# Kernel tuning notes

Measured on AMD Instinct MI355X. Metric: run time of the kernel, lower is better.

Reference implementation:

```python
import jax, jax.numpy as jnp
import numpy as np

CW = 32            # correlationWidth (number of disparities)
HR = 3             # horizontalCorrelationRadius
VR = 3             # verticalCorrelationRadius
EPS = 1e-09        # normalizationEpsilon
KH, KW = 2 * VR + 1, 2 * HR + 1  # unfold kernel (7,7)

B, C, H, W = 2, 16, 128, 256


def _unfold_patches(img):
    # img: [b,c,h,w] -> [b, c*KH*KW, h, w'] ('same' padding, like nn.Unfold with padding=(3,3)).
    # Feature-dim ordering differs from torch's unfold but NCC is invariant to it
    # (mean / norm / dot all reduce over the full patch dim).
    return jax.lax.conv_general_dilated_patches(
        img, (KH, KW), (1, 1), [(VR, VR), (HR, HR)])


def _normalize_patches(p):
    # zero-mean, unit-L2 per patch (reduce over feature dim 1)
    p = p - p.mean(axis=1, keepdims=True)
    return p / jnp.sqrt(jnp.sum(p * p, axis=1, keepdims=True) + EPS)


def setup_inputs() -> dict:
    key = jax.random.key(0)
    k1, k2 = jax.random.split(key)
    im_left = jax.random.normal(k1, (B, C, H, W), dtype=jnp.float32)
    im_right = jax.random.normal(k2, (B, C, H, W), dtype=jnp.float32)
    return {"im_left": im_left, "im_right": im_right}


def reference(im_left, im_right):
    b, c, h, w = im_left.shape
    # ZeroPad2d((0, CW-1, 0, 0)): pad right edge of width by CW-1 zeros
    left_ext = jnp.pad(im_left, ((0, 0), (0, 0), (0, 0), (0, CW - 1)))
    pl = _normalize_patches(_unfold_patches(left_ext))   # [b,P,h,w+CW-1]
    pr = _normalize_patches(_unfold_patches(im_right))   # [b,P,h,w]
    # cost[b,y,x,d] = <normalized left patch at (y, x+d), normalized right patch at (y, x)>
    cost = jnp.stack(
        [jnp.einsum('bpyx,bpyx->byx', pl[..., d:d + w], pr) for d in range(CW)],
        axis=-1)  # [b,h,w,CW]
    return cost
```

## Files before the change

kernel.cpp:

```cpp
#include <hip/hip_runtime.h>

#define NB 2
#define NC 16
#define NH 128
#define NW 256
#define NCW 32
#define HW (NH*NW)
#define PATCH_INV (1.0f/784.0f)
#define EPS_N 1e-9f
#define HB_W 272

__global__ __launch_bounds__(256) void ncc_kernel(
    const float* __restrict__ L, const float* __restrict__ R, float* __restrict__ out)
{
    __shared__ float csL[NW], cs2L[NW], csR[NW], cs2R[NW];
    __shared__ float sSL[288], sInvL[288], sSR[NW], sInvR[NW];
    __shared__ float hbuf[NCW][HB_W];

    const int bid = blockIdx.x;
    const int lin = (bid & 7) * 32 + (bid >> 3);
    const int b = lin >> 7;
    const int y = lin & 127;

    const int t  = threadIdx.x;
    const int dq = t >> 6;
    const int xg = t & 63;
    const int x0 = xg << 2;
    const int d0 = dq << 3;
    const int s  = x0 + d0;

    const size_t base = (size_t)b * NC * HW;

    {
        float aL = 0.f, a2L = 0.f, aR = 0.f, a2R = 0.f;
        #pragma unroll
        for (int dy = -3; dy <= 3; ++dy) {
            int yy = y + dy;
            if ((unsigned)yy < NH) {
                const float* lp = L + base + (size_t)yy * NW + t;
                const float* rp = R + base + (size_t)yy * NW + t;
                #pragma unroll
                for (int c = 0; c < NC; ++c) {
                    float lv = lp[c * HW];
                    float rv = rp[c * HW];
                    aL += lv; a2L += lv * lv;
                    aR += rv; a2R += rv * rv;
                }
            }
        }
        csL[t] = aL; cs2L[t] = a2L; csR[t] = aR; cs2R[t] = a2R;
    }
    __syncthreads();

    #pragma unroll
    for (int rep = 0; rep < 2; ++rep) {
        int xe = t + rep * 256;
        if (xe < 288) {
            float S = 0.f, S2 = 0.f;
            #pragma unroll
            for (int dx = -3; dx <= 3; ++dx) {
                int xx = xe + dx;
                if ((unsigned)xx < NW) { S += csL[xx]; S2 += cs2L[xx]; }
            }
            sSL[xe]   = S;
            sInvL[xe] = rsqrtf(S2 - S * S * PATCH_INV + EPS_N);
        }
    }
    {
        float S = 0.f, S2 = 0.f;
        #pragma unroll
        for (int dx = -3; dx <= 3; ++dx) {
            int xx = t + dx;
            if ((unsigned)xx < NW) { S += csR[xx]; S2 += cs2R[xx]; }
        }
        sSR[t]   = S;
        sInvR[t] = rsqrtf(S2 - S * S * PATCH_INV + EPS_N);
    }
    __syncthreads();

    float vp[4][8];
    #pragma unroll
    for (int i = 0; i < 4; ++i)
        #pragma unroll
        for (int j = 0; j < 8; ++j) vp[i][j] = 0.f;

    #pragma unroll
    for (int dy = -3; dy <= 3; ++dy) {
        const int yy = y + dy;
        if ((unsigned)yy < NH) {
            const float* lrow = L + base + (size_t)yy * NW;
            const float* rrow = R + base + (size_t)yy * NW;
            #pragma unroll
            for (int c = 0; c < NC; ++c) {
                const float* lc = lrow + (size_t)c * HW;
                const float* rc = rrow + (size_t)c * HW;
                float4 rv4 = *(const float4*)(rc + x0);
                float rv[4] = {rv4.x, rv4.y, rv4.z, rv4.w};
                float lw[12];
                #pragma unroll
                for (int ch = 0; ch < 3; ++ch) {
                    int col  = s + ch * 4;
                    int colc = col < (NW - 4) ? col : (NW - 4);
                    float4 lv = *(const float4*)(lc + colc);
                    bool ok = (col < NW);
                    lw[ch*4+0] = ok ? lv.x : 0.f;
                    lw[ch*4+1] = ok ? lv.y : 0.f;
                    lw[ch*4+2] = ok ? lv.z : 0.f;
                    lw[ch*4+3] = ok ? lv.w : 0.f;
                }
                #pragma unroll
                for (int xx = 0; xx < 4; ++xx)
                    #pragma unroll
                    for (int j = 0; j < 8; ++j)
                        vp[xx][j] += lw[xx + j] * rv[xx];
            }
        }
    }
    #pragma unroll
    for (int j = 0; j < 8; ++j)
        *(float4*)&hbuf[d0 + j][4 + x0] =
            make_float4(vp[0][j], vp[1][j], vp[2][j], vp[3][j]);
    if (t < 128) {
        int r = t >> 2, q = t & 3;
        int col = (q == 0) ? 0 : (260 + 4 * (q - 1));
        *(float4*)&hbuf[r][col] = make_float4(0.f, 0.f, 0.f, 0.f);
    }
    __syncthreads();

    float res[4][8];
    #pragma unroll
    for (int j = 0; j < 8; ++j) {
        float4 w0 = *(float4*)&hbuf[d0+j][x0];
        float4 w1 = *(float4*)&hbuf[d0+j][x0+4];
        float4 w2 = *(float4*)&hbuf[d0+j][x0+8];
        float w[12] = {w0.x,w0.y,w0.z,w0.w, w1.x,w1.y,w1.z,w1.w, w2.x,w2.y,w2.z,w2.w};
        #pragma unroll
        for (int xx = 0; xx < 4; ++xx) {
            float sum = 0.f;
            #pragma unroll
            for (int k = 1; k <= 7; ++k) sum += w[xx + k];
            float slv = sSL[s + xx + j];
            float ilv = sInvL[s + xx + j];
            float srv = sSR[x0 + xx];
            float irv = sInvR[x0 + xx];
            res[xx][j] = (sum - slv * srv * PATCH_INV) * ilv * irv;
        }
    }

    float* op = out + (((size_t)(b * NH + y) * NW) + x0) * NCW + d0;
    #pragma unroll
    for (int xx = 0; xx < 4; ++xx) {
        *(float4*)(op + (size_t)xx * NCW)     =
            make_float4(res[xx][0], res[xx][1], res[xx][2], res[xx][3]);
        *(float4*)(op + (size_t)xx * NCW + 4) =
            make_float4(res[xx][4], res[xx][5], res[xx][6], res[xx][7]);
    }
}

extern "C" void kernel_launch(void* const* d_in, const int* in_sizes, int n_in,
                              void* d_out, int out_size, void* d_ws, size_t ws_size,
                              hipStream_t stream) {
    const float* L = (const float*)d_in[0];
    const float* R = (const float*)d_in[1];
    float* out = (float*)d_out;
    ncc_kernel<<<dim3(NB * NH), dim3(256), 0, stream>>>(L, R, out);
}
```

Measured before the change: 84.79 us.

## Double threads per block, each computing 4 disparities instead of 8

Blocks grow to 512 threads, and each thread now handles 4 disparities per 4 x-positions instead of 8. The box-sum prologue is split so that half the threads cover the left image and half the right. This raises the number of waves per block for 256 blocks on a large GPU, giving better latency hiding and fewer registers per thread. The cost is more redundant global loads of the left and right rows per disparity group and a larger block that may limit residency.

```diff
diff --git a/kernel.cpp b/kernel.cpp
--- a/kernel.cpp
+++ b/kernel.cpp
@@ -10,7 +10,7 @@
 #define EPS_N 1e-9f
 #define HB_W 272
 
-__global__ __launch_bounds__(256) void ncc_kernel(
+__global__ __launch_bounds__(512) void ncc_kernel(
     const float* __restrict__ L, const float* __restrict__ R, float* __restrict__ out)
 {
     __shared__ float csL[NW], cs2L[NW], csR[NW], cs2R[NW];
@@ -26,63 +26,60 @@
     const int dq = t >> 6;
     const int xg = t & 63;
     const int x0 = xg << 2;
-    const int d0 = dq << 3;
+    const int d0 = dq << 2;
     const int s  = x0 + d0;
 
     const size_t base = (size_t)b * NC * HW;
 
     {
-        float aL = 0.f, a2L = 0.f, aR = 0.f, a2R = 0.f;
+        const float* img = (t < 256) ? L : R;
+        const int col = t & 255;
+        float a = 0.f, a2 = 0.f;
         #pragma unroll
         for (int dy = -3; dy <= 3; ++dy) {
             int yy = y + dy;
             if ((unsigned)yy < NH) {
-                const float* lp = L + base + (size_t)yy * NW + t;
-                const float* rp = R + base + (size_t)yy * NW + t;
+                const float* p = img + base + (size_t)yy * NW + col;
                 #pragma unroll
                 for (int c = 0; c < NC; ++c) {
-                    float lv = lp[c * HW];
-                    float rv = rp[c * HW];
-                    aL += lv; a2L += lv * lv;
-                    aR += rv; a2R += rv * rv;
+                    float v = p[c * HW];
+                    a += v; a2 += v * v;
                 }
             }
         }
-        csL[t] = aL; cs2L[t] = a2L; csR[t] = aR; cs2R[t] = a2R;
+        if (t < 256) { csL[col] = a; cs2L[col] = a2; }
+        else         { csR[col] = a; cs2R[col] = a2; }
     }
     __syncthreads();
 
-    #pragma unroll
-    for (int rep = 0; rep < 2; ++rep) {
-        int xe = t + rep * 256;
-        if (xe < 288) {
-            float S = 0.f, S2 = 0.f;
-            #pragma unroll
-            for (int dx = -3; dx <= 3; ++dx) {
-                int xx = xe + dx;
-                if ((unsigned)xx < NW) { S += csL[xx]; S2 += cs2L[xx]; }
-            }
-            sSL[xe]   = S;
-            sInvL[xe] = rsqrtf(S2 - S * S * PATCH_INV + EPS_N);
-        }
-    }
-    {
+    if (t < 288) {
         float S = 0.f, S2 = 0.f;
         #pragma unroll
         for (int dx = -3; dx <= 3; ++dx) {
             int xx = t + dx;
+            if ((unsigned)xx < NW) { S += csL[xx]; S2 += cs2L[xx]; }
+        }
+        sSL[t]   = S;
+        sInvL[t] = rsqrtf(S2 - S * S * PATCH_INV + EPS_N);
+    }
+    if (t >= 256) {
+        const int xr = t - 256;
+        float S = 0.f, S2 = 0.f;
+        #pragma unroll
+        for (int dx = -3; dx <= 3; ++dx) {
+            int xx = xr + dx;
             if ((unsigned)xx < NW) { S += csR[xx]; S2 += cs2R[xx]; }
         }
-        sSR[t]   = S;
-        sInvR[t] = rsqrtf(S2 - S * S * PATCH_INV + EPS_N);
+        sSR[xr]   = S;
+        sInvR[xr] = rsqrtf(S2 - S * S * PATCH_INV + EPS_N);
     }
     __syncthreads();
 
-    float vp[4][8];
+    float vp[4][4];
     #pragma unroll
     for (int i = 0; i < 4; ++i)
         #pragma unroll
-        for (int j = 0; j < 8; ++j) vp[i][j] = 0.f;
+        for (int j = 0; j < 4; ++j) vp[i][j] = 0.f;
 
     #pragma unroll
     for (int dy = -3; dy <= 3; ++dy) {
@@ -96,9 +93,9 @@
                 const float* rc = rrow + (size_t)c * HW;
                 float4 rv4 = *(const float4*)(rc + x0);
                 float rv[4] = {rv4.x, rv4.y, rv4.z, rv4.w};
-                float lw[12];
+                float lw[8];
                 #pragma unroll
-                for (int ch = 0; ch < 3; ++ch) {
+                for (int ch = 0; ch < 2; ++ch) {
                     int col  = s + ch * 4;
                     int colc = col < (NW - 4) ? col : (NW - 4);
                     float4 lv = *(const float4*)(lc + colc);
@@ -111,13 +108,13 @@
                 #pragma unroll
                 for (int xx = 0; xx < 4; ++xx)
                     #pragma unroll
-                    for (int j = 0; j < 8; ++j)
+                    for (int j = 0; j < 4; ++j)
                         vp[xx][j] += lw[xx + j] * rv[xx];
             }
         }
     }
     #pragma unroll
-    for (int j = 0; j < 8; ++j)
+    for (int j = 0; j < 4; ++j)
         *(float4*)&hbuf[d0 + j][4 + x0] =
             make_float4(vp[0][j], vp[1][j], vp[2][j], vp[3][j]);
     if (t < 128) {
@@ -127,9 +124,9 @@
     }
     __syncthreads();
 
-    float res[4][8];
+    float res[4][4];
     #pragma unroll
-    for (int j = 0; j < 8; ++j) {
+    for (int j = 0; j < 4; ++j) {
         float4 w0 = *(float4*)&hbuf[d0+j][x0];
         float4 w1 = *(float4*)&hbuf[d0+j][x0+4];
         float4 w2 = *(float4*)&hbuf[d0+j][x0+8];
@@ -149,12 +146,9 @@
 
     float* op = out + (((size_t)(b * NH + y) * NW) + x0) * NCW + d0;
     #pragma unroll
-    for (int xx = 0; xx < 4; ++xx) {
-        *(float4*)(op + (size_t)xx * NCW)     =
+    for (int xx = 0; xx < 4; ++xx)
+        *(float4*)(op + (size_t)xx * NCW) =
             make_float4(res[xx][0], res[xx][1], res[xx][2], res[xx][3]);
-        *(float4*)(op + (size_t)xx * NCW + 4) =
-            make_float4(res[xx][4], res[xx][5], res[xx][6], res[xx][7]);
-    }
 }
 
 extern "C" void kernel_launch(void* const* d_in, const int* in_sizes, int n_in,
@@ -163,5 +157,5 @@
     const float* L = (const float*)d_in[0];
     const float* R = (const float*)d_in[1];
     float* out = (float*)d_out;
-    ncc_kernel<<<dim3(NB * NH), dim3(256), 0, stream>>>(L, R, out);
+    ncc_kernel<<<dim3(NB * NH), dim3(512), 0, stream>>>(L, R, out);
 }
```

Result: slower. 87.08 us (+2.7%).

## Split patch-stat pass across threads with float4 loads and branchless row clamping

Applied to the files above, without the earlier changes.

The first pass over the image, which builds column sums and squared sums, is repartitioned. Each thread now handles one image, half of the 7 vertical taps and 4 columns using float4 loads, and the partial results are combined through a new shared-memory buffer with an extra barrier. Both the stats loop and the main correlation loop replace the per-row boundary branch with a clamped row index and a 0/1 mask multiply, so the loops unroll fully with no branches. Launch bounds now request a minimum of one block per multiprocessor. The cost is wasted loads on masked edge rows, a little more shared memory and one more synchronisation.

```diff
diff --git a/kernel.cpp b/kernel.cpp
--- a/kernel.cpp
+++ b/kernel.cpp
@@ -10,9 +10,10 @@
 #define EPS_N 1e-9f
 #define HB_W 272
 
-__global__ __launch_bounds__(256) void ncc_kernel(
+__global__ __launch_bounds__(256, 1) void ncc_kernel(
     const float* __restrict__ L, const float* __restrict__ R, float* __restrict__ out)
 {
+    __shared__ float psum[2][2][64][8];
     __shared__ float csL[NW], cs2L[NW], csR[NW], cs2R[NW];
     __shared__ float sSL[288], sInvL[288], sSR[NW], sInvR[NW];
     __shared__ float hbuf[NCW][HB_W];
@@ -32,23 +33,42 @@
     const size_t base = (size_t)b * NC * HW;
 
     {
-        float aL = 0.f, a2L = 0.f, aR = 0.f, a2R = 0.f;
+        const int img = t >> 7;
+        const int dyh = (t >> 6) & 1;
+        const int q   = t & 63;
+        const float* I = img ? R : L;
+        const int dy0 = dyh ? 4 : 0;
+        const int ndy = dyh ? 3 : 4;
+        float s0=0.f,s1=0.f,s2v=0.f,s3=0.f, q0=0.f,q1=0.f,q2=0.f,q3=0.f;
         #pragma unroll
-        for (int dy = -3; dy <= 3; ++dy) {
-            int yy = y + dy;
-            if ((unsigned)yy < NH) {
-                const float* lp = L + base + (size_t)yy * NW + t;
-                const float* rp = R + base + (size_t)yy * NW + t;
+        for (int k = 0; k < 4; ++k) {
+            if (k < ndy) {
+                const int yy  = y - 3 + dy0 + k;
+                const int yyc = yy < 0 ? 0 : (yy > NH - 1 ? NH - 1 : yy);
+                const float m = ((unsigned)yy < NH) ? 1.f : 0.f;
+                const float* p = I + base + (size_t)yyc * NW + (q << 2);
                 #pragma unroll
                 for (int c = 0; c < NC; ++c) {
-                    float lv = lp[c * HW];
-                    float rv = rp[c * HW];
-                    aL += lv; a2L += lv * lv;
-                    aR += rv; a2R += rv * rv;
+                    float4 v = *(const float4*)(p + (size_t)c * HW);
+                    float a0 = m * v.x, a1 = m * v.y, a2 = m * v.z, a3 = m * v.w;
+                    s0 += a0; s1 += a1; s2v += a2; s3 += a3;
+                    q0 += a0 * v.x; q1 += a1 * v.y; q2 += a2 * v.z; q3 += a3 * v.w;
                 }
             }
         }
-        csL[t] = aL; cs2L[t] = a2L; csR[t] = aR; cs2R[t] = a2R;
+        psum[img][dyh][q][0] = s0; psum[img][dyh][q][1] = s1;
+        psum[img][dyh][q][2] = s2v; psum[img][dyh][q][3] = s3;
+        psum[img][dyh][q][4] = q0; psum[img][dyh][q][5] = q1;
+        psum[img][dyh][q][6] = q2; psum[img][dyh][q][7] = q3;
+    }
+    __syncthreads();
+
+    {
+        const int q = t >> 2, r = t & 3;
+        csL[t]  = psum[0][0][q][r]     + psum[0][1][q][r];
+        cs2L[t] = psum[0][0][q][r + 4] + psum[0][1][q][r + 4];
+        csR[t]  = psum[1][0][q][r]     + psum[1][1][q][r];
+        cs2R[t] = psum[1][0][q][r + 4] + psum[1][1][q][r + 4];
     }
     __syncthreads();
 
@@ -85,35 +105,35 @@
         for (int j = 0; j < 8; ++j) vp[i][j] = 0.f;
 
     #pragma unroll
-    for (int dy = -3; dy <= 3; ++dy) {
-        const int yy = y + dy;
-        if ((unsigned)yy < NH) {
-            const float* lrow = L + base + (size_t)yy * NW;
-            const float* rrow = R + base + (size_t)yy * NW;
+    for (int k = 0; k < 7; ++k) {
+        const int yy  = y - 3 + k;
+        const int yyc = yy < 0 ? 0 : (yy > NH - 1 ? NH - 1 : yy);
+        const float rm = ((unsigned)yy < NH) ? 1.f : 0.f;
+        const float* lrow = L + base + (size_t)yyc * NW;
+        const float* rrow = R + base + (size_t)yyc * NW;
+        #pragma unroll
+        for (int c = 0; c < NC; ++c) {
+            const float* lc = lrow + (size_t)c * HW;
+            const float* rc = rrow + (size_t)c * HW;
+            float4 rv4 = *(const float4*)(rc + x0);
+            float rv[4] = {rm * rv4.x, rm * rv4.y, rm * rv4.z, rm * rv4.w};
+            float lw[12];
             #pragma unroll
-            for (int c = 0; c < NC; ++c) {
-                const float* lc = lrow + (size_t)c * HW;
-                const float* rc = rrow + (size_t)c * HW;
-                float4 rv4 = *(const float4*)(rc + x0);
-                float rv[4] = {rv4.x, rv4.y, rv4.z, rv4.w};
-                float lw[12];
+            for (int ch = 0; ch < 3; ++ch) {
+                int col  = s + ch * 4;
+                int colc = col < (NW - 4) ? col : (NW - 4);
+                float4 lv = *(const float4*)(lc + colc);
+                bool ok = (col < NW);
+                lw[ch*4+0] = ok ? lv.x : 0.f;
+                lw[ch*4+1] = ok ? lv.y : 0.f;
+                lw[ch*4+2] = ok ? lv.z : 0.f;
+                lw[ch*4+3] = ok ? lv.w : 0.f;
+            }
+            #pragma unroll
+            for (int xx = 0; xx < 4; ++xx)
                 #pragma unroll
-                for (int ch = 0; ch < 3; ++ch) {
-                    int col  = s + ch * 4;
-                    int colc = col < (NW - 4) ? col : (NW - 4);
-                    float4 lv = *(const float4*)(lc + colc);
-                    bool ok = (col < NW);
-                    lw[ch*4+0] = ok ? lv.x : 0.f;
-                    lw[ch*4+1] = ok ? lv.y : 0.f;
-                    lw[ch*4+2] = ok ? lv.z : 0.f;
-                    lw[ch*4+3] = ok ? lv.w : 0.f;
-                }
-                #pragma unroll
-                for (int xx = 0; xx < 4; ++xx)
-                    #pragma unroll
-                    for (int j = 0; j < 8; ++j)
-                        vp[xx][j] += lw[xx + j] * rv[xx];
-            }
+                for (int j = 0; j < 8; ++j)
+                    vp[xx][j] += lw[xx + j] * rv[xx];
         }
     }
     #pragma unroll
```

After: 159.5 us. +88.1%, slower.
